# Kernel optimization log

Measured on AMD Instinct MI355X. Metric: run time of the kernel, lower is better.

Reference implementation:

```python
import jax, jax.numpy as jnp
import numpy as np

D, H, F, E, K = 1024, 16, 2048, 8, 2
EPS = 1e-5


def layernorm(x, g, b):
    m = jnp.mean(x, axis=-1, keepdims=True)
    v = jnp.mean((x - m) ** 2, axis=-1, keepdims=True)
    return (x - m) * jax.lax.rsqrt(v + EPS) * g + b


def mha(q_in, k_in, v_in, wq, wk, wv, bq, bk, bv, wo, bo):
    B, Tq, Dm = q_in.shape
    Tk = k_in.shape[1]
    dh = Dm // H
    q = (q_in @ wq + bq).reshape(B, Tq, H, dh)
    k = (k_in @ wk + bk).reshape(B, Tk, H, dh)
    v = (v_in @ wv + bv).reshape(B, Tk, H, dh)
    scores = jnp.einsum('bqhd,bkhd->bhqk', q, k) / jnp.sqrt(jnp.asarray(dh, q.dtype))
    attn = jax.nn.softmax(scores, axis=-1)
    out = jnp.einsum('bhqk,bkhd->bqhd', attn, v).reshape(B, Tq, Dm)
    return out @ wo + bo


def moe(x, rw, rb, w1, b1, w2, b2):
    B, T, Dm = x.shape
    xt = x.reshape(-1, Dm)                      # [N, D]
    N = xt.shape[0]
    logits = xt @ rw + rb                       # [N, E]
    probs = jax.nn.softmax(logits, axis=-1)
    topv, topi = jax.lax.top_k(probs, K)        # [N, K]
    gates = topv / jnp.sum(topv, axis=-1, keepdims=True)
    dense_gates = jnp.zeros((N, E), x.dtype).at[jnp.arange(N)[:, None], topi].set(gates)
    h = jax.nn.relu(jnp.einsum('td,edf->etf', xt, w1) + b1[:, None, :])  # [E, N, F]
    y = jnp.einsum('etf,efd->etd', h, w2) + b2[:, None, :]               # [E, N, D]
    out = jnp.einsum('te,etd->td', dense_gates, y).reshape(B, T, Dm)
    frac = jnp.mean(jnp.sum(jax.nn.one_hot(topi, E, dtype=x.dtype), axis=1) / K, axis=0)  # [E]
    importance = jnp.mean(probs, axis=0)        # [E]
    lb_loss = E * jnp.sum(frac * importance)
    return out, lb_loss


def forward(tgt, memory,
            sa_wq, sa_wk, sa_wv, sa_bq, sa_bk, sa_bv, sa_wo, sa_bo,
            ca_wq, ca_wk, ca_wv, ca_bq, ca_bk, ca_bv, ca_wo, ca_bo,
            ln1_g, ln1_b, ln2_g, ln2_b, ln3_g, ln3_b,
            rw, rb, w1, b1, w2, b2):
    t2 = mha(tgt, tgt, tgt, sa_wq, sa_wk, sa_wv, sa_bq, sa_bk, sa_bv, sa_wo, sa_bo)
    t = layernorm(tgt + t2, ln1_g, ln1_b)
    t2 = mha(t, memory, memory, ca_wq, ca_wk, ca_wv, ca_bq, ca_bk, ca_bv, ca_wo, ca_bo)
    t = layernorm(t + t2, ln2_g, ln2_b)
    t2, lb = moe(t, rw, rb, w1, b1, w2, b2)
    t = layernorm(t + t2, ln3_g, ln3_b)
    return t, lb


def setup_inputs() -> dict:
    key = jax.random.key(0)
    ks = jax.random.split(key, 24)
    s = 1.0 / np.sqrt(D)
    inp = {
        'tgt': jax.random.normal(ks[0], (4, 512, D), jnp.float32),
        'memory': jax.random.normal(ks[1], (4, 512, D), jnp.float32),
    }
    names = ['sa_wq', 'sa_wk', 'sa_wv', 'sa_wo', 'ca_wq', 'ca_wk', 'ca_wv', 'ca_wo']
    for i, n in enumerate(names):
        inp[n] = jax.random.normal(ks[2 + i], (D, D), jnp.float32) * s
    for n in ['sa_bq', 'sa_bk', 'sa_bv', 'sa_bo', 'ca_bq', 'ca_bk', 'ca_bv', 'ca_bo']:
        inp[n] = jnp.zeros((D,), jnp.float32)
    for n in ['ln1_g', 'ln2_g', 'ln3_g']:
        inp[n] = jnp.ones((D,), jnp.float32)
    for n in ['ln1_b', 'ln2_b', 'ln3_b']:
        inp[n] = jnp.zeros((D,), jnp.float32)
    inp['rw'] = jax.random.normal(ks[10], (D, E), jnp.float32) * s
    inp['rb'] = jnp.zeros((E,), jnp.float32)
    inp['w1'] = jax.random.normal(ks[11], (E, D, F), jnp.float32) * s
    inp['b1'] = jnp.zeros((E, F), jnp.float32)
    inp['w2'] = jax.random.normal(ks[12], (E, F, D), jnp.float32) * (1.0 / np.sqrt(F))
    inp['b2'] = jnp.zeros((E, D), jnp.float32)
    return inp


def reference(tgt, memory,
              sa_wq, sa_wk, sa_wv, sa_bq, sa_bk, sa_bv, sa_wo, sa_bo,
              ca_wq, ca_wk, ca_wv, ca_bq, ca_bk, ca_bv, ca_wo, ca_bo,
              ln1_g, ln1_b, ln2_g, ln2_b, ln3_g, ln3_b,
              rw, rb, w1, b1, w2, b2):
    return forward(tgt, memory,
                   sa_wq, sa_wk, sa_wv, sa_bq, sa_bk, sa_bv, sa_wo, sa_bo,
                   ca_wq, ca_wk, ca_wv, ca_bq, ca_bk, ca_bv, ca_wo, ca_bo,
                   ln1_g, ln1_b, ln2_g, ln2_b, ln3_g, ln3_b,
                   rw, rb, w1, b1, w2, b2)
```

## Files before the change

kernel.cpp:

```cpp
#include <hip/hip_runtime.h>

constexpr int Dm = 1024;
constexpr int NH = 16;
constexpr int Ff = 2048;
constexpr int NE = 8;
constexpr int Bn = 4;
constexpr int Tn = 512;
constexpr int Nt = 2048;

typedef float  f32x4  __attribute__((ext_vector_type(4)));
typedef __bf16 bf16x8 __attribute__((ext_vector_type(8)));
typedef unsigned short u16x8 __attribute__((ext_vector_type(8)));

__device__ inline unsigned short f2bf(float f) {
    unsigned u = __builtin_bit_cast(unsigned, f);
    u += 0x7FFFu + ((u >> 16) & 1u);
    return (unsigned short)(u >> 16);
}
__device__ inline float bf2f(unsigned short h) {
    unsigned u = (unsigned)h << 16;
    return __builtin_bit_cast(float, u);
}
__device__ inline void splitbf(float x, unsigned short& hi, unsigned short& lo) {
    hi = f2bf(x);
    lo = f2bf(x - bf2f(hi));
}
__device__ inline bf16x8 ld_frag(const unsigned short* p) {
    return __builtin_bit_cast(bf16x8, *(const u16x8*)p);
}

template <int SPLIT>
__global__ __launch_bounds__(256) void gemm_bf16_kernel(
    const float* __restrict__ A, int lda,
    const float* __restrict__ W0, const float* __restrict__ W1,
    const float* __restrict__ W2, int ldw, size_t weStride,
    const float* __restrict__ B0, const float* __restrict__ B1,
    const float* __restrict__ B2, size_t beStride,
    float* __restrict__ C, int ldc,
    int Mparam, int K,
    const int* __restrict__ lst, int lstStride, const int* __restrict__ cnt,
    int mode, int relu)
{
    __shared__ __align__(16) unsigned short AsH[128 * 40];
    __shared__ __align__(16) unsigned short WsH[128 * 40];
    __shared__ __align__(16) unsigned short AsL[SPLIT ? 128 * 40 : 1];
    __shared__ __align__(16) unsigned short WsL[SPLIT ? 128 * 40 : 1];
    __shared__ int inIdx[128];
    __shared__ int outIdx[128];

    const int e = blockIdx.z;
    const int M = (mode == 0) ? Mparam : cnt[e];
    const int m0 = blockIdx.y * 128;
    if (m0 >= M) return;
    const int n0 = blockIdx.x * 128;
    const int seg = n0 >> 10;
    const float* W = ((seg == 0) ? W0 : (seg == 1) ? W1 : W2) + (size_t)e * weStride;
    const float* bias = ((seg == 0) ? B0 : (seg == 1) ? B1 : B2) + (size_t)e * beStride;
    const int nseg = n0 & 1023;
    const int tid = threadIdx.x;

    if (tid < 128) {
        int g = m0 + tid;
        bool valid = g < M;
        int gi, go;
        if (mode == 0) { gi = valid ? g : (M - 1); go = valid ? g : -1; }
        else {
            int pid = lst[(size_t)e * lstStride + (valid ? g : 0)];
            gi = (mode == 1) ? (pid >> 1) : pid;
            go = valid ? pid : -1;
        }
        inIdx[tid] = gi;
        outIdx[tid] = go;
    }
    __syncthreads();

    const int ar = tid >> 1, ahalf = tid & 1;
    const int bn = (tid & 63) * 2, bko = ((tid >> 6) & 3) * 8;
    const float* aBase = A + (size_t)inIdx[ar] * lda + ahalf * 16;
    const float* wBase = W + (size_t)bko * ldw + nseg + bn;

    const int lane = tid & 63, wv = tid >> 6;
    const int wy = (wv >> 1) * 64, wx = (wv & 1) * 64;
    const int l15 = lane & 15, quad = lane >> 4;

    f32x4 acc[4][4];
    #pragma unroll
    for (int i = 0; i < 4; ++i)
        #pragma unroll
        for (int j = 0; j < 4; ++j) acc[i][j] = (f32x4)0.f;

    for (int k0 = 0; k0 < K; k0 += 32) {
        {
            const float* ap = aBase + k0;
            float v[16];
            *(float4*)&v[0]  = *(const float4*)(ap);
            *(float4*)&v[4]  = *(const float4*)(ap + 4);
            *(float4*)&v[8]  = *(const float4*)(ap + 8);
            *(float4*)&v[12] = *(const float4*)(ap + 12);
            u16x8 h0, h1, l0, l1;
            #pragma unroll
            for (int i = 0; i < 8; ++i) {
                unsigned short hh, ll;
                splitbf(v[i], hh, ll); h0[i] = hh; l0[i] = ll;
                splitbf(v[8 + i], hh, ll); h1[i] = hh; l1[i] = ll;
            }
            *(u16x8*)&AsH[ar * 40 + ahalf * 16]     = h0;
            *(u16x8*)&AsH[ar * 40 + ahalf * 16 + 8] = h1;
            if (SPLIT) {
                *(u16x8*)&AsL[ar * 40 + ahalf * 16]     = l0;
                *(u16x8*)&AsL[ar * 40 + ahalf * 16 + 8] = l1;
            }
        }
        {
            const float* wp = wBase + (size_t)k0 * ldw;
            float2 wr[8];
            #pragma unroll
            for (int j = 0; j < 8; ++j) wr[j] = *(const float2*)(wp + (size_t)j * ldw);
            u16x8 h0, h1, l0, l1;
            #pragma unroll
            for (int j = 0; j < 8; ++j) {
                unsigned short hh, ll;
                splitbf(wr[j].x, hh, ll); h0[j] = hh; l0[j] = ll;
                splitbf(wr[j].y, hh, ll); h1[j] = hh; l1[j] = ll;
            }
            *(u16x8*)&WsH[bn * 40 + bko]       = h0;
            *(u16x8*)&WsH[(bn + 1) * 40 + bko] = h1;
            if (SPLIT) {
                *(u16x8*)&WsL[bn * 40 + bko]       = l0;
                *(u16x8*)&WsL[(bn + 1) * 40 + bko] = l1;
            }
        }
        __syncthreads();
        bf16x8 ah[4], bh[4], al[4], bl[4];
        #pragma unroll
        for (int mi = 0; mi < 4; ++mi)
            ah[mi] = ld_frag(&AsH[(wy + mi * 16 + l15) * 40 + quad * 8]);
        #pragma unroll
        for (int ni = 0; ni < 4; ++ni)
            bh[ni] = ld_frag(&WsH[(wx + ni * 16 + l15) * 40 + quad * 8]);
        if (SPLIT) {
            #pragma unroll
            for (int mi = 0; mi < 4; ++mi)
                al[mi] = ld_frag(&AsL[(wy + mi * 16 + l15) * 40 + quad * 8]);
            #pragma unroll
            for (int ni = 0; ni < 4; ++ni)
                bl[ni] = ld_frag(&WsL[(wx + ni * 16 + l15) * 40 + quad * 8]);
        }
        #pragma unroll
        for (int mi = 0; mi < 4; ++mi)
            #pragma unroll
            for (int ni = 0; ni < 4; ++ni) {
                acc[mi][ni] = __builtin_amdgcn_mfma_f32_16x16x32_bf16(
                    ah[mi], bh[ni], acc[mi][ni], 0, 0, 0);
                if (SPLIT) {
                    acc[mi][ni] = __builtin_amdgcn_mfma_f32_16x16x32_bf16(
                        ah[mi], bl[ni], acc[mi][ni], 0, 0, 0);
                    acc[mi][ni] = __builtin_amdgcn_mfma_f32_16x16x32_bf16(
                        al[mi], bh[ni], acc[mi][ni], 0, 0, 0);
                }
            }
        __syncthreads();
    }

    #pragma unroll
    for (int mi = 0; mi < 4; ++mi) {
        #pragma unroll
        for (int r = 0; r < 4; ++r) {
            int rl = wy + mi * 16 + quad * 4 + r;
            int orow = outIdx[rl];
            if (orow < 0) continue;
            #pragma unroll
            for (int ni = 0; ni < 4; ++ni) {
                int col = n0 + wx + ni * 16 + l15;
                float val = acc[mi][ni][r] + bias[col & 1023];
                if (relu) val = fmaxf(val, 0.f);
                C[(size_t)orow * ldc + col] = val;
            }
        }
    }
}

__global__ __launch_bounds__(256) void attn_kernel(
    const float* __restrict__ Qp, int qld,
    const float* __restrict__ Kp, int kld, int kOff,
    const float* __restrict__ Vp, int vld, int vOff,
    float* __restrict__ O)
{
    __shared__ __align__(16) unsigned short KtH[64 * 72], KtL[64 * 72];
    __shared__ __align__(16) unsigned short VtH[64 * 72], VtL[64 * 72];
    __shared__ __align__(16) unsigned short PtH[4][16 * 72], PtL[4][16 * 72];

    const int tid = threadIdx.x, lane = tid & 63, wv = tid >> 6;
    const int quad = lane >> 4, l15 = lane & 15;
    const int b = blockIdx.z, h = blockIdx.y, q0 = blockIdx.x * 64;
    const int bT = b * Tn;

    bf16x8 aqh[2], aql[2];
    {
        const float* qp = Qp + (size_t)(bT + q0 + wv * 16 + l15) * qld + h * 64;
        #pragma unroll
        for (int s = 0; s < 2; ++s) {
            float v[8];
            *(float4*)&v[0] = *(const float4*)(qp + s * 32 + quad * 8);
            *(float4*)&v[4] = *(const float4*)(qp + s * 32 + quad * 8 + 4);
            u16x8 th, tl;
            #pragma unroll
            for (int i = 0; i < 8; ++i) {
                unsigned short hh, ll;
                splitbf(v[i], hh, ll); th[i] = hh; tl[i] = ll;
            }
            aqh[s] = __builtin_bit_cast(bf16x8, th);
            aql[s] = __builtin_bit_cast(bf16x8, tl);
        }
    }

    f32x4 oacc[4];
    #pragma unroll
    for (int i = 0; i < 4; ++i) oacc[i] = (f32x4)0.f;
    float mrow[4] = {-1e30f, -1e30f, -1e30f, -1e30f};
    float lrow[4] = {0.f, 0.f, 0.f, 0.f};

    const int rr = tid >> 2, cc = tid & 3;

    for (int kt0 = 0; kt0 < Tn; kt0 += 64) {
        {
            const float* kr = Kp + (size_t)(bT + kt0 + rr) * kld + kOff + h * 64 + cc * 16;
            float v[16];
            *(float4*)&v[0]  = *(const float4*)(kr);
            *(float4*)&v[4]  = *(const float4*)(kr + 4);
            *(float4*)&v[8]  = *(const float4*)(kr + 8);
            *(float4*)&v[12] = *(const float4*)(kr + 12);
            u16x8 h0, h1, l0, l1;
            #pragma unroll
            for (int i = 0; i < 8; ++i) {
                unsigned short hh, ll;
                splitbf(v[i], hh, ll); h0[i] = hh; l0[i] = ll;
                splitbf(v[8 + i], hh, ll); h1[i] = hh; l1[i] = ll;
            }
            *(u16x8*)&KtH[rr * 72 + cc * 16]     = h0;
            *(u16x8*)&KtH[rr * 72 + cc * 16 + 8] = h1;
            *(u16x8*)&KtL[rr * 72 + cc * 16]     = l0;
            *(u16x8*)&KtL[rr * 72 + cc * 16 + 8] = l1;

            const float* vr = Vp + (size_t)(bT + kt0 + rr) * vld + vOff + h * 64 + cc * 16;
            float fv[16];
            *(float4*)&fv[0]  = *(const float4*)(vr);
            *(float4*)&fv[4]  = *(const float4*)(vr + 4);
            *(float4*)&fv[8]  = *(const float4*)(vr + 8);
            *(float4*)&fv[12] = *(const float4*)(vr + 12);
            #pragma unroll
            for (int i = 0; i < 16; ++i) {
                unsigned short hh, ll;
                splitbf(fv[i], hh, ll);
                VtH[(cc * 16 + i) * 72 + rr] = hh;
                VtL[(cc * 16 + i) * 72 + rr] = ll;
            }
        }
        __syncthreads();

        f32x4 sacc[4];
        #pragma unroll
        for (int nt = 0; nt < 4; ++nt) {
            sacc[nt] = (f32x4)0.f;
            #pragma unroll
            for (int s = 0; s < 2; ++s) {
                bf16x8 bkh = ld_frag(&KtH[(nt * 16 + l15) * 72 + s * 32 + quad * 8]);
                bf16x8 bkl = ld_frag(&KtL[(nt * 16 + l15) * 72 + s * 32 + quad * 8]);
                sacc[nt] = __builtin_amdgcn_mfma_f32_16x16x32_bf16(aqh[s], bkh, sacc[nt], 0, 0, 0);
                sacc[nt] = __builtin_amdgcn_mfma_f32_16x16x32_bf16(aqh[s], bkl, sacc[nt], 0, 0, 0);
                sacc[nt] = __builtin_amdgcn_mfma_f32_16x16x32_bf16(aql[s], bkh, sacc[nt], 0, 0, 0);
            }
        }
        #pragma unroll
        for (int nt = 0; nt < 4; ++nt)
            #pragma unroll
            for (int r = 0; r < 4; ++r) sacc[nt][r] *= 0.125f;

        float alpha[4], mnew[4];
        #pragma unroll
        for (int r = 0; r < 4; ++r) {
            float mx = fmaxf(fmaxf(sacc[0][r], sacc[1][r]), fmaxf(sacc[2][r], sacc[3][r]));
            #pragma unroll
            for (int msk = 1; msk < 16; msk <<= 1) mx = fmaxf(mx, __shfl_xor(mx, msk));
            mnew[r] = fmaxf(mrow[r], mx);
            alpha[r] = __expf(mrow[r] - mnew[r]);
            mrow[r] = mnew[r];
        }
        float rs[4] = {0.f, 0.f, 0.f, 0.f};
        #pragma unroll
        for (int nt = 0; nt < 4; ++nt)
            #pragma unroll
            for (int r = 0; r < 4; ++r) {
                float p = __expf(sacc[nt][r] - mnew[r]);
                sacc[nt][r] = p;
                rs[r] += p;
            }
        #pragma unroll
        for (int r = 0; r < 4; ++r) {
            #pragma unroll
            for (int msk = 1; msk < 16; msk <<= 1) rs[r] += __shfl_xor(rs[r], msk);
            lrow[r] = lrow[r] * alpha[r] + rs[r];
        }
        #pragma unroll
        for (int ni = 0; ni < 4; ++ni)
            #pragma unroll
            for (int r = 0; r < 4; ++r) oacc[ni][r] *= alpha[r];

        #pragma unroll
        for (int nt = 0; nt < 4; ++nt)
            #pragma unroll
            for (int r = 0; r < 4; ++r) {
                unsigned short hh, ll;
                splitbf(sacc[nt][r], hh, ll);
                PtH[wv][(quad * 4 + r) * 72 + nt * 16 + l15] = hh;
                PtL[wv][(quad * 4 + r) * 72 + nt * 16 + l15] = ll;
            }
        asm volatile("s_waitcnt lgkmcnt(0)" ::: "memory");

        #pragma unroll
        for (int s = 0; s < 2; ++s) {
            bf16x8 aph = ld_frag(&PtH[wv][l15 * 72 + s * 32 + quad * 8]);
            bf16x8 apl = ld_frag(&PtL[wv][l15 * 72 + s * 32 + quad * 8]);
            #pragma unroll
            for (int ni = 0; ni < 4; ++ni) {
                bf16x8 bvh = ld_frag(&VtH[(ni * 16 + l15) * 72 + s * 32 + quad * 8]);
                bf16x8 bvl = ld_frag(&VtL[(ni * 16 + l15) * 72 + s * 32 + quad * 8]);
                oacc[ni] = __builtin_amdgcn_mfma_f32_16x16x32_bf16(aph, bvh, oacc[ni], 0, 0, 0);
                oacc[ni] = __builtin_amdgcn_mfma_f32_16x16x32_bf16(aph, bvl, oacc[ni], 0, 0, 0);
                oacc[ni] = __builtin_amdgcn_mfma_f32_16x16x32_bf16(apl, bvh, oacc[ni], 0, 0, 0);
            }
        }
        __syncthreads();
    }

    #pragma unroll
    for (int r = 0; r < 4; ++r) {
        float inv = 1.f / lrow[r];
        int orow = bT + q0 + wv * 16 + quad * 4 + r;
        #pragma unroll
        for (int ni = 0; ni < 4; ++ni) {
            int col = h * 64 + ni * 16 + l15;
            O[(size_t)orow * Dm + col] = oacc[ni][r] * inv;
        }
    }
}

__global__ __launch_bounds__(256) void ln_residual_kernel(
    const float* __restrict__ X, const float* __restrict__ R,
    const float* __restrict__ g, const float* __restrict__ bta,
    float* __restrict__ Out)
{
    __shared__ float red[8];
    const int t = blockIdx.x, tid = threadIdx.x;
    float v[4];
    float s = 0.f;
    #pragma unroll
    for (int i = 0; i < 4; ++i) {
        int c = tid + i * 256;
        v[i] = X[(size_t)t * Dm + c] + R[(size_t)t * Dm + c];
        s += v[i];
    }
    #pragma unroll
    for (int off = 32; off; off >>= 1) s += __shfl_down(s, off);
    const int wid = tid >> 6;
    if ((tid & 63) == 0) red[wid] = s;
    __syncthreads();
    const float mean = (red[0] + red[1] + red[2] + red[3]) * (1.f / 1024.f);
    float s2 = 0.f;
    #pragma unroll
    for (int i = 0; i < 4; ++i) { float d = v[i] - mean; s2 += d * d; }
    #pragma unroll
    for (int off = 32; off; off >>= 1) s2 += __shfl_down(s2, off);
    if ((tid & 63) == 0) red[4 + wid] = s2;
    __syncthreads();
    const float var  = (red[4] + red[5] + red[6] + red[7]) * (1.f / 1024.f);
    const float rstd = rsqrtf(var + 1e-5f);
    #pragma unroll
    for (int i = 0; i < 4; ++i) {
        int c = tid + i * 256;
        Out[(size_t)t * Dm + c] = (v[i] - mean) * rstd * g[c] + bta[c];
    }
}

constexpr int RT_TPB = 32;
__global__ __launch_bounds__(256) void router_kernel(
    const float* __restrict__ X, const float* __restrict__ rw,
    const float* __restrict__ rb, float* __restrict__ gatep,
    int* __restrict__ elist, int* __restrict__ ecnt,
    float* __restrict__ impf, float* __restrict__ cntf)
{
    __shared__ float simp[NE];
    __shared__ int   scnt[NE];
    __shared__ int   sbase[NE];
    __shared__ int   sexp[RT_TPB][2];
    __shared__ int   spos[RT_TPB][2];

    const int tid = threadIdx.x, lane = tid & 63, wv = tid >> 6;
    if (tid < NE) { simp[tid] = 0.f; scnt[tid] = 0; }
    __syncthreads();

    const int t0 = blockIdx.x * RT_TPB;

    for (int i = 0; i < 8; ++i) {
        const int slot = wv * 8 + i;
        const int t = t0 + slot;
        float l[NE];
        #pragma unroll
        for (int e = 0; e < NE; ++e) l[e] = 0.f;
        #pragma unroll
        for (int j = 0; j < Dm / 64; ++j) {
            int d = lane + j * 64;
            float x = X[(size_t)t * Dm + d];
            #pragma unroll
            for (int e = 0; e < NE; ++e) l[e] += x * rw[d * NE + e];
        }
        #pragma unroll
        for (int e = 0; e < NE; ++e) {
            float vv = l[e];
            #pragma unroll
            for (int off = 32; off; off >>= 1) vv += __shfl_down(vv, off);
            l[e] = vv;
        }
        if (lane == 0) {
            float mx = -1e30f;
            #pragma unroll
            for (int e = 0; e < NE; ++e) { l[e] += rb[e]; mx = fmaxf(mx, l[e]); }
            float p[NE];
            float sum = 0.f;
            #pragma unroll
            for (int e = 0; e < NE; ++e) { p[e] = __expf(l[e] - mx); sum += p[e]; }
            const float inv = 1.f / sum;
            int e0 = 0, e1 = 0;
            float v0 = -1.f, v1 = -1.f;
            #pragma unroll
            for (int e = 0; e < NE; ++e) {
                float pe = p[e] * inv;
                atomicAdd(&simp[e], pe);
                if (pe > v0)      { v1 = v0; e1 = e0; v0 = pe; e0 = e; }
                else if (pe > v1) { v1 = pe; e1 = e; }
            }
            const float gs = 1.f / (v0 + v1);
            sexp[slot][0] = e0;
            sexp[slot][1] = e1;
            spos[slot][0] = atomicAdd(&scnt[e0], 1);
            spos[slot][1] = atomicAdd(&scnt[e1], 1);
            gatep[2 * t]     = v0 * gs;
            gatep[2 * t + 1] = v1 * gs;
        }
    }
    __syncthreads();

    if (tid < NE) {
        sbase[tid] = atomicAdd(&ecnt[tid], scnt[tid]);
        atomicAdd(&impf[tid], simp[tid]);
        atomicAdd(&cntf[tid], (float)scnt[tid]);
    }
    __syncthreads();

    if (tid < RT_TPB * 2) {
        const int slot = tid >> 1, k = tid & 1;
        const int e = sexp[slot][k];
        elist[e * Nt + sbase[e] + spos[slot][k]] = 2 * (t0 + slot) + k;
    }
}

__global__ void init_kernel(int* ecnt, float* impf, float* cntf)
{
    int i = threadIdx.x;
    if (i < NE) { ecnt[i] = 0; impf[i] = 0.f; cntf[i] = 0.f; }
}

__global__ void lb_kernel(const float* __restrict__ impf,
                          const float* __restrict__ cntf,
                          float* __restrict__ out)
{
    if (threadIdx.x == 0) {
        float s = 0.f;
        for (int e = 0; e < NE; ++e) s += cntf[e] * impf[e];
        out[0] = (float)NE * s / ((float)Nt * 2.f * (float)Nt);
    }
}

__global__ __launch_bounds__(256) void moe_combine(
    const float* __restrict__ Y, const float* __restrict__ gatep,
    float* __restrict__ Out)
{
    int i = blockIdx.x * 256 + threadIdx.x;
    int t = i >> 10, c = i & 1023;
    Out[i] = gatep[2 * t] * Y[(size_t)(2 * t) * Dm + c]
           + gatep[2 * t + 1] * Y[(size_t)(2 * t + 1) * Dm + c];
}

extern "C" void kernel_launch(void* const* d_in, const int* in_sizes, int n_in,
                              void* d_out, int out_size, void* d_ws, size_t ws_size,
                              hipStream_t stream)
{
    const float* tgt   = (const float*)d_in[0];
    const float* memry = (const float*)d_in[1];
    const float* sa_wq = (const float*)d_in[2];
    const float* sa_wk = (const float*)d_in[3];
    const float* sa_wv = (const float*)d_in[4];
    const float* sa_wo = (const float*)d_in[5];
    const float* ca_wq = (const float*)d_in[6];
    const float* ca_wk = (const float*)d_in[7];
    const float* ca_wv = (const float*)d_in[8];
    const float* ca_wo = (const float*)d_in[9];
    const float* sa_bq = (const float*)d_in[10];
    const float* sa_bk = (const float*)d_in[11];
    const float* sa_bv = (const float*)d_in[12];
    const float* sa_bo = (const float*)d_in[13];
    const float* ca_bq = (const float*)d_in[14];
    const float* ca_bk = (const float*)d_in[15];
    const float* ca_bv = (const float*)d_in[16];
    const float* ca_bo = (const float*)d_in[17];
    const float* ln1_g = (const float*)d_in[18];
    const float* ln2_g = (const float*)d_in[19];
    const float* ln3_g = (const float*)d_in[20];
    const float* ln1_b = (const float*)d_in[21];
    const float* ln2_b = (const float*)d_in[22];
    const float* ln3_b = (const float*)d_in[23];
    const float* rw    = (const float*)d_in[24];
    const float* rb    = (const float*)d_in[25];
    const float* w1    = (const float*)d_in[26];
    const float* b1    = (const float*)d_in[27];
    const float* w2    = (const float*)d_in[28];
    const float* b2    = (const float*)d_in[29];

    float* ws = (float*)d_ws;
    const size_t ND = (size_t)Nt * Dm;
    float* qkv  = ws;
    float* qc   = ws;
    float* kvc  = ws + ND;
    float* attnO = ws + 3 * ND;
    float* hbuf = ws;
    float* t2   = ws + 4 * ND;
    float* tb   = ws + 5 * ND;
    float* ybuf = ws + 6 * ND;
    float* gatep = ws + 8 * ND;
    int*   elist = (int*)(gatep + 2 * Nt);
    int*   ecnt  = elist + NE * Nt;
    float* impf  = (float*)(ecnt + NE);
    float* cntf  = impf + NE;
    float* outp  = (float*)d_out;

    dim3 blk(256);
    dim3 attnGrid(Tn / 64, NH, Bn);

    gemm_bf16_kernel<1><<<dim3(24, 16, 1), blk, 0, stream>>>(
        tgt, Dm, sa_wq, sa_wk, sa_wv, Dm, 0, sa_bq, sa_bk, sa_bv, 0,
        qkv, 3 * Dm, Nt, Dm, nullptr, 0, nullptr, 0, 0);
    attn_kernel<<<attnGrid, blk, 0, stream>>>(
        qkv, 3 * Dm, qkv, 3 * Dm, 1024, qkv, 3 * Dm, 2048, attnO);
    gemm_bf16_kernel<1><<<dim3(8, 16, 1), blk, 0, stream>>>(
        attnO, Dm, sa_wo, sa_wo, sa_wo, Dm, 0, sa_bo, sa_bo, sa_bo, 0,
        t2, Dm, Nt, Dm, nullptr, 0, nullptr, 0, 0);
    ln_residual_kernel<<<Nt, blk, 0, stream>>>(tgt, t2, ln1_g, ln1_b, tb);

    gemm_bf16_kernel<1><<<dim3(8, 16, 1), blk, 0, stream>>>(
        tb, Dm, ca_wq, ca_wq, ca_wq, Dm, 0, ca_bq, ca_bq, ca_bq, 0,
        qc, Dm, Nt, Dm, nullptr, 0, nullptr, 0, 0);
    gemm_bf16_kernel<1><<<dim3(16, 16, 1), blk, 0, stream>>>(
        memry, Dm, ca_wk, ca_wv, ca_wv, Dm, 0, ca_bk, ca_bv, ca_bv, 0,
        kvc, 2 * Dm, Nt, Dm, nullptr, 0, nullptr, 0, 0);
    attn_kernel<<<attnGrid, blk, 0, stream>>>(
        qc, Dm, kvc, 2 * Dm, 0, kvc, 2 * Dm, 1024, attnO);
    gemm_bf16_kernel<1><<<dim3(8, 16, 1), blk, 0, stream>>>(
        attnO, Dm, ca_wo, ca_wo, ca_wo, Dm, 0, ca_bo, ca_bo, ca_bo, 0,
        t2, Dm, Nt, Dm, nullptr, 0, nullptr, 0, 0);
    ln_residual_kernel<<<Nt, blk, 0, stream>>>(tb, t2, ln2_g, ln2_b, tb);

    init_kernel<<<1, 64, 0, stream>>>(ecnt, impf, cntf);
    router_kernel<<<Nt / RT_TPB, blk, 0, stream>>>(tb, rw, rb, gatep, elist, ecnt, impf, cntf);
    gemm_bf16_kernel<1><<<dim3(16, 16, 8), blk, 0, stream>>>(
        tb, Dm, w1, w1 + 1024, w1 + 1024, Ff, (size_t)Dm * Ff, b1, b1 + 1024, b1 + 1024, Ff,
        hbuf, Ff, 0, Dm, elist, Nt, ecnt, 1, 1);
    gemm_bf16_kernel<1><<<dim3(8, 16, 8), blk, 0, stream>>>(
        hbuf, Ff, w2, w2, w2, Dm, (size_t)Ff * Dm, b2, b2, b2, Dm,
        ybuf, Dm, 0, Ff, elist, Nt, ecnt, 2, 0);
    moe_combine<<<(Nt * Dm) / 256, blk, 0, stream>>>(ybuf, gatep, t2);
    ln_residual_kernel<<<Nt, blk, 0, stream>>>(tb, t2, ln3_g, ln3_b, outp);
    lb_kernel<<<1, 64, 0, stream>>>(impf, cntf, outp + ND);
}
```

Measured before the change: 896.0 us.

## Pre-split operands to bf16 hi/lo, use direct LDS loads, fuse MoE combine

```diff
diff --git a/kernel.cpp b/kernel.cpp
--- a/kernel.cpp
+++ b/kernel.cpp
@@ -10,41 +10,52 @@
 
 typedef float  f32x4  __attribute__((ext_vector_type(4)));
 typedef __bf16 bf16x8 __attribute__((ext_vector_type(8)));
-typedef unsigned short u16x8 __attribute__((ext_vector_type(8)));
-
-__device__ inline unsigned short f2bf(float f) {
+typedef unsigned short u16;
+typedef u16 u16x8v __attribute__((ext_vector_type(8)));
+typedef u16 u16x4v __attribute__((ext_vector_type(4)));
+
+__device__ inline u16 f2bf(float f) {
     unsigned u = __builtin_bit_cast(unsigned, f);
     u += 0x7FFFu + ((u >> 16) & 1u);
-    return (unsigned short)(u >> 16);
-}
-__device__ inline float bf2f(unsigned short h) {
+    return (u16)(u >> 16);
+}
+__device__ inline float bf2f(u16 h) {
     unsigned u = (unsigned)h << 16;
     return __builtin_bit_cast(float, u);
 }
-__device__ inline void splitbf(float x, unsigned short& hi, unsigned short& lo) {
+__device__ inline void splitbf(float x, u16& hi, u16& lo) {
     hi = f2bf(x);
     lo = f2bf(x - bf2f(hi));
 }
-__device__ inline bf16x8 ld_frag(const unsigned short* p) {
-    return __builtin_bit_cast(bf16x8, *(const u16x8*)p);
-}
-
-template <int SPLIT>
-__global__ __launch_bounds__(256) void gemm_bf16_kernel(
-    const float* __restrict__ A, int lda,
-    const float* __restrict__ W0, const float* __restrict__ W1,
-    const float* __restrict__ W2, int ldw, size_t weStride,
+__device__ inline bf16x8 ld_frag(const u16* p) {
+    return __builtin_bit_cast(bf16x8, *(const u16x8v*)p);
+}
+__device__ inline void cp16(const u16* g, u16* l) {
+    __builtin_amdgcn_global_load_lds(
+        (const __attribute__((address_space(1))) unsigned int*)g,
+        (__attribute__((address_space(3))) unsigned int*)l, 16, 0, 0);
+}
+
+template <int SPLIT, int CMODE>
+__global__ __launch_bounds__(256) void gemm_kernel(
+    const u16* __restrict__ Ahi, const u16* __restrict__ Alo, int lda,
+    const u16* __restrict__ Whi, const u16* __restrict__ Wlo, size_t weStride,
     const float* __restrict__ B0, const float* __restrict__ B1,
     const float* __restrict__ B2, size_t beStride,
-    float* __restrict__ C, int ldc,
+    void* __restrict__ C0, void* __restrict__ C1, int ldc,
     int Mparam, int K,
     const int* __restrict__ lst, int lstStride, const int* __restrict__ cnt,
-    int mode, int relu)
-{
-    __shared__ __align__(16) unsigned short AsH[128 * 40];
-    __shared__ __align__(16) unsigned short WsH[128 * 40];
-    __shared__ __align__(16) unsigned short AsL[SPLIT ? 128 * 40 : 1];
-    __shared__ __align__(16) unsigned short WsL[SPLIT ? 128 * 40 : 1];
+    int mode, int relu,
+    const u16* __restrict__ A2hi, const u16* __restrict__ A2lo, int lda2,
+    const u16* __restrict__ W2hi, const u16* __restrict__ W2lo,
+    const float* __restrict__ B20, const float* __restrict__ B21,
+    void* __restrict__ C20, void* __restrict__ C21, int ldc2, int xSplit,
+    const float* __restrict__ gatep, float* __restrict__ accOut)
+{
+    __shared__ __align__(16) u16 AsH[128 * 32];
+    __shared__ __align__(16) u16 WsH[128 * 32];
+    __shared__ __align__(16) u16 AsL[SPLIT ? 128 * 32 : 8];
+    __shared__ __align__(16) u16 WsL[SPLIT ? 128 * 32 : 8];
     __shared__ int inIdx[128];
     __shared__ int outIdx[128];
 
@@ -52,11 +63,21 @@
     const int M = (mode == 0) ? Mparam : cnt[e];
     const int m0 = blockIdx.y * 128;
     if (m0 >= M) return;
-    const int n0 = blockIdx.x * 128;
-    const int seg = n0 >> 10;
-    const float* W = ((seg == 0) ? W0 : (seg == 1) ? W1 : W2) + (size_t)e * weStride;
-    const float* bias = ((seg == 0) ? B0 : (seg == 1) ? B1 : B2) + (size_t)e * beStride;
-    const int nseg = n0 & 1023;
+
+    int bx = blockIdx.x;
+    const u16 *aH = Ahi, *aL = Alo, *wH = Whi, *wL = Wlo;
+    const float *b0 = B0, *b1 = B1, *b2 = B2;
+    void *c0 = C0, *c1 = C1;
+    int myLda = lda, myLdc = ldc;
+    if (xSplit && bx >= xSplit) {
+        bx -= xSplit;
+        aH = A2hi; aL = A2lo; wH = W2hi; wL = W2lo;
+        b0 = B20; b1 = B21; b2 = B21;
+        c0 = C20; c1 = C21; myLda = lda2; myLdc = ldc2;
+    }
+    const int n0 = bx * 128;
+    const int seg = n0 >> 10, nseg = n0 & 1023;
+    const float* bias = ((seg == 0) ? b0 : (seg == 1) ? b1 : b2) + (size_t)e * beStride;
     const int tid = threadIdx.x;
 
     if (tid < 128) {
@@ -74,12 +95,32 @@
     }
     __syncthreads();
 
-    const int ar = tid >> 1, ahalf = tid & 1;
-    const int bn = (tid & 63) * 2, bko = ((tid >> 6) & 3) * 8;
-    const float* aBase = A + (size_t)inIdx[ar] * lda + ahalf * 16;
-    const float* wBase = W + (size_t)bko * ldw + nseg + bn;
-
     const int lane = tid & 63, wv = tid >> 6;
+    const int c0i = wv * 2, c1i = wv * 2 + 1;
+    const int r0 = c0i * 16 + (lane >> 2), r1 = c1i * 16 + (lane >> 2);
+    const int kc0 = (lane & 3) ^ ((r0 >> 1) & 3);
+    const int kc1 = (lane & 3) ^ ((r1 >> 1) & 3);
+    const size_t wOff = (size_t)e * weStride;
+    const u16* aH0 = aH + (size_t)inIdx[r0] * myLda + kc0 * 8;
+    const u16* aH1 = aH + (size_t)inIdx[r1] * myLda + kc1 * 8;
+    const u16* wH0 = wH + wOff + (size_t)(n0 + r0) * K + kc0 * 8;
+    const u16* wH1 = wH + wOff + (size_t)(n0 + r1) * K + kc1 * 8;
+    const u16 *aL0 = nullptr, *aL1 = nullptr, *wL0 = nullptr, *wL1 = nullptr;
+    if (SPLIT) {
+        aL0 = aL + (size_t)inIdx[r0] * myLda + kc0 * 8;
+        aL1 = aL + (size_t)inIdx[r1] * myLda + kc1 * 8;
+        wL0 = wL + wOff + (size_t)(n0 + r0) * K + kc0 * 8;
+        wL1 = wL + wOff + (size_t)(n0 + r1) * K + kc1 * 8;
+    }
+    u16* ldsA0 = &AsH[c0i * 512];
+    u16* ldsA1 = &AsH[c1i * 512];
+    u16* ldsW0 = &WsH[c0i * 512];
+    u16* ldsW1 = &WsH[c1i * 512];
+    u16* ldsAL0 = SPLIT ? &AsL[c0i * 512] : nullptr;
+    u16* ldsAL1 = SPLIT ? &AsL[c1i * 512] : nullptr;
+    u16* ldsWL0 = SPLIT ? &WsL[c0i * 512] : nullptr;
+    u16* ldsWL1 = SPLIT ? &WsL[c1i * 512] : nullptr;
+
     const int wy = (wv >> 1) * 64, wx = (wv & 1) * 64;
     const int l15 = lane & 15, quad = lane >> 4;
 
@@ -90,61 +131,32 @@
         for (int j = 0; j < 4; ++j) acc[i][j] = (f32x4)0.f;
 
     for (int k0 = 0; k0 < K; k0 += 32) {
-        {
-            const float* ap = aBase + k0;
-            float v[16];
-            *(float4*)&v[0]  = *(const float4*)(ap);
-            *(float4*)&v[4]  = *(const float4*)(ap + 4);
-            *(float4*)&v[8]  = *(const float4*)(ap + 8);
-            *(float4*)&v[12] = *(const float4*)(ap + 12);
-            u16x8 h0, h1, l0, l1;
-            #pragma unroll
-            for (int i = 0; i < 8; ++i) {
-                unsigned short hh, ll;
-                splitbf(v[i], hh, ll); h0[i] = hh; l0[i] = ll;
-                splitbf(v[8 + i], hh, ll); h1[i] = hh; l1[i] = ll;
-            }
-            *(u16x8*)&AsH[ar * 40 + ahalf * 16]     = h0;
-            *(u16x8*)&AsH[ar * 40 + ahalf * 16 + 8] = h1;
-            if (SPLIT) {
-                *(u16x8*)&AsL[ar * 40 + ahalf * 16]     = l0;
-                *(u16x8*)&AsL[ar * 40 + ahalf * 16 + 8] = l1;
-            }
-        }
-        {
-            const float* wp = wBase + (size_t)k0 * ldw;
-            float2 wr[8];
-            #pragma unroll
-            for (int j = 0; j < 8; ++j) wr[j] = *(const float2*)(wp + (size_t)j * ldw);
-            u16x8 h0, h1, l0, l1;
-            #pragma unroll
-            for (int j = 0; j < 8; ++j) {
-                unsigned short hh, ll;
-                splitbf(wr[j].x, hh, ll); h0[j] = hh; l0[j] = ll;
-                splitbf(wr[j].y, hh, ll); h1[j] = hh; l1[j] = ll;
-            }
-            *(u16x8*)&WsH[bn * 40 + bko]       = h0;
-            *(u16x8*)&WsH[(bn + 1) * 40 + bko] = h1;
-            if (SPLIT) {
-                *(u16x8*)&WsL[bn * 40 + bko]       = l0;
-                *(u16x8*)&WsL[(bn + 1) * 40 + bko] = l1;
-            }
+        cp16(aH0 + k0, ldsA0);
+        cp16(aH1 + k0, ldsA1);
+        cp16(wH0 + k0, ldsW0);
+        cp16(wH1 + k0, ldsW1);
+        if (SPLIT) {
+            cp16(aL0 + k0, ldsAL0);
+            cp16(aL1 + k0, ldsAL1);
+            cp16(wL0 + k0, ldsWL0);
+            cp16(wL1 + k0, ldsWL1);
         }
         __syncthreads();
+
         bf16x8 ah[4], bh[4], al[4], bl[4];
         #pragma unroll
-        for (int mi = 0; mi < 4; ++mi)
-            ah[mi] = ld_frag(&AsH[(wy + mi * 16 + l15) * 40 + quad * 8]);
-        #pragma unroll
-        for (int ni = 0; ni < 4; ++ni)
-            bh[ni] = ld_frag(&WsH[(wx + ni * 16 + l15) * 40 + quad * 8]);
-        if (SPLIT) {
-            #pragma unroll
-            for (int mi = 0; mi < 4; ++mi)
-                al[mi] = ld_frag(&AsL[(wy + mi * 16 + l15) * 40 + quad * 8]);
-            #pragma unroll
-            for (int ni = 0; ni < 4; ++ni)
-                bl[ni] = ld_frag(&WsL[(wx + ni * 16 + l15) * 40 + quad * 8]);
+        for (int mi = 0; mi < 4; ++mi) {
+            int r = wy + mi * 16 + l15;
+            int sl = quad ^ ((r >> 1) & 3);
+            ah[mi] = ld_frag(&AsH[r * 32 + sl * 8]);
+            if (SPLIT) al[mi] = ld_frag(&AsL[r * 32 + sl * 8]);
+        }
+        #pragma unroll
+        for (int ni = 0; ni < 4; ++ni) {
+            int r = wx + ni * 16 + l15;
+            int sl = quad ^ ((r >> 1) & 3);
+            bh[ni] = ld_frag(&WsH[r * 32 + sl * 8]);
+            if (SPLIT) bl[ni] = ld_frag(&WsL[r * 32 + sl * 8]);
         }
         #pragma unroll
         for (int mi = 0; mi < 4; ++mi)
@@ -171,24 +183,37 @@
             if (orow < 0) continue;
             #pragma unroll
             for (int ni = 0; ni < 4; ++ni) {
-                int col = n0 + wx + ni * 16 + l15;
-                float val = acc[mi][ni][r] + bias[col & 1023];
+                int col = nseg + wx + ni * 16 + l15;
+                float val = acc[mi][ni][r] + bias[col];
                 if (relu) val = fmaxf(val, 0.f);
-                C[(size_t)orow * ldc + col] = val;
+                int gcol = n0 + wx + ni * 16 + l15;
+                if (CMODE == 3) {
+                    atomicAdd(&accOut[(size_t)(orow >> 1) * Dm + gcol],
+                              gatep[orow] * val);
+                } else if (CMODE == 2) {
+                    u16 hh, ll;
+                    splitbf(val, hh, ll);
+                    ((u16*)c0)[(size_t)orow * myLdc + gcol] = hh;
+                    ((u16*)c1)[(size_t)orow * myLdc + gcol] = ll;
+                } else if (CMODE == 1) {
+                    ((u16*)c0)[(size_t)orow * myLdc + gcol] = f2bf(val);
+                } else {
+                    ((float*)c0)[(size_t)orow * myLdc + gcol] = val;
+                }
             }
         }
     }
 }
 
 __global__ __launch_bounds__(256) void attn_kernel(
-    const float* __restrict__ Qp, int qld,
-    const float* __restrict__ Kp, int kld, int kOff,
-    const float* __restrict__ Vp, int vld, int vOff,
-    float* __restrict__ O)
-{
-    __shared__ __align__(16) unsigned short KtH[64 * 72], KtL[64 * 72];
-    __shared__ __align__(16) unsigned short VtH[64 * 72], VtL[64 * 72];
-    __shared__ __align__(16) unsigned short PtH[4][16 * 72], PtL[4][16 * 72];
+    const u16* __restrict__ QH, const u16* __restrict__ QL, int qld, int qOff,
+    const u16* __restrict__ KH, const u16* __restrict__ KL, int kld, int kOff,
+    const u16* __restrict__ VH, const u16* __restrict__ VL, int vld, int vOff,
+    u16* __restrict__ OH, u16* __restrict__ OL)
+{
+    __shared__ __align__(16) u16 KtH[64 * 72], KtL[64 * 72];
+    __shared__ __align__(16) u16 VtH[64 * 72], VtL[64 * 72];
+    __shared__ __align__(16) u16 PtH[4][16 * 72], PtL[4][16 * 72];
 
     const int tid = threadIdx.x, lane = tid & 63, wv = tid >> 6;
     const int quad = lane >> 4, l15 = lane & 15;
@@ -197,20 +222,11 @@
 
     bf16x8 aqh[2], aql[2];
     {
-        const float* qp = Qp + (size_t)(bT + q0 + wv * 16 + l15) * qld + h * 64;
+        size_t qbase = (size_t)(bT + q0 + wv * 16 + l15) * qld + qOff + h * 64;
         #pragma unroll
         for (int s = 0; s < 2; ++s) {
-            float v[8];
-            *(float4*)&v[0] = *(const float4*)(qp + s * 32 + quad * 8);
-            *(float4*)&v[4] = *(const float4*)(qp + s * 32 + quad * 8 + 4);
-            u16x8 th, tl;
-            #pragma unroll
-            for (int i = 0; i < 8; ++i) {
-                unsigned short hh, ll;
-                splitbf(v[i], hh, ll); th[i] = hh; tl[i] = ll;
-            }
-            aqh[s] = __builtin_bit_cast(bf16x8, th);
-            aql[s] = __builtin_bit_cast(bf16x8, tl);
+            aqh[s] = ld_frag(QH + qbase + s * 32 + quad * 8);
+            aql[s] = ld_frag(QL + qbase + s * 32 + quad * 8);
         }
     }
 
@@ -224,36 +240,23 @@
 
     for (int kt0 = 0; kt0 < Tn; kt0 += 64) {
         {
-            const float* kr = Kp + (size_t)(bT + kt0 + rr) * kld + kOff + h * 64 + cc * 16;
-            float v[16];
-            *(float4*)&v[0]  = *(const float4*)(kr);
-            *(float4*)&v[4]  = *(const float4*)(kr + 4);
-            *(float4*)&v[8]  = *(const float4*)(kr + 8);
-            *(float4*)&v[12] = *(const float4*)(kr + 12);
-            u16x8 h0, h1, l0, l1;
+            size_t kb = (size_t)(bT + kt0 + rr) * kld + kOff + h * 64 + cc * 16;
+            *(u16x8v*)&KtH[rr * 72 + cc * 16]     = *(const u16x8v*)(KH + kb);
+            *(u16x8v*)&KtH[rr * 72 + cc * 16 + 8] = *(const u16x8v*)(KH + kb + 8);
+            *(u16x8v*)&KtL[rr * 72 + cc * 16]     = *(const u16x8v*)(KL + kb);
+            *(u16x8v*)&KtL[rr * 72 + cc * 16 + 8] = *(const u16x8v*)(KL + kb + 8);
+
+            size_t vb = (size_t)(bT + kt0 + rr) * vld + vOff + h * 64 + cc * 16;
+            u16x8v va = *(const u16x8v*)(VH + vb);
+            u16x8v vbv = *(const u16x8v*)(VH + vb + 8);
+            u16x8v la = *(const u16x8v*)(VL + vb);
+            u16x8v lb = *(const u16x8v*)(VL + vb + 8);
             #pragma unroll
             for (int i = 0; i < 8; ++i) {
-                unsigned short hh, ll;
-                splitbf(v[i], hh, ll); h0[i] = hh; l0[i] = ll;
-                splitbf(v[8 + i], hh, ll); h1[i] = hh; l1[i] = ll;
-            }
-            *(u16x8*)&KtH[rr * 72 + cc * 16]     = h0;
-            *(u16x8*)&KtH[rr * 72 + cc * 16 + 8] = h1;
-            *(u16x8*)&KtL[rr * 72 + cc * 16]     = l0;
-            *(u16x8*)&KtL[rr * 72 + cc * 16 + 8] = l1;
-
-            const float* vr = Vp + (size_t)(bT + kt0 + rr) * vld + vOff + h * 64 + cc * 16;
-            float fv[16];
-            *(float4*)&fv[0]  = *(const float4*)(vr);
-            *(float4*)&fv[4]  = *(const float4*)(vr + 4);
-            *(float4*)&fv[8]  = *(const float4*)(vr + 8);
-            *(float4*)&fv[12] = *(const float4*)(vr + 12);
-            #pragma unroll
-            for (int i = 0; i < 16; ++i) {
-                unsigned short hh, ll;
-                splitbf(fv[i], hh, ll);
-                VtH[(cc * 16 + i) * 72 + rr] = hh;
-                VtL[(cc * 16 + i) * 72 + rr] = ll;
+                VtH[(cc * 16 + i) * 72 + rr]     = va[i];
+                VtH[(cc * 16 + 8 + i) * 72 + rr] = vbv[i];
+                VtL[(cc * 16 + i) * 72 + rr]     = la[i];
+                VtL[(cc * 16 + 8 + i) * 72 + rr] = lb[i];
             }
         }
         __syncthreads();
@@ -310,7 +313,7 @@
         for (int nt = 0; nt < 4; ++nt)
             #pragma unroll
             for (int r = 0; r < 4; ++r) {
-                unsigned short hh, ll;
+                u16 hh, ll;
                 splitbf(sacc[nt][r], hh, ll);
                 PtH[wv][(quad * 4 + r) * 72 + nt * 16 + l15] = hh;
                 PtL[wv][(quad * 4 + r) * 72 + nt * 16 + l15] = ll;
@@ -340,7 +343,10 @@
         #pragma unroll
         for (int ni = 0; ni < 4; ++ni) {
             int col = h * 64 + ni * 16 + l15;
-            O[(size_t)orow * Dm + col] = oacc[ni][r] * inv;
+            u16 hh, ll;
+            splitbf(oacc[ni][r] * inv, hh, ll);
+            OH[(size_t)orow * Dm + col] = hh;
+            OL[(size_t)orow * Dm + col] = ll;
         }
     }
 }
@@ -348,7 +354,7 @@
 __global__ __launch_bounds__(256) void ln_residual_kernel(
     const float* __restrict__ X, const float* __restrict__ R,
     const float* __restrict__ g, const float* __restrict__ bta,
-    float* __restrict__ Out)
+    float* __restrict__ Out, u16* __restrict__ outH, u16* __restrict__ outL)
 {
     __shared__ float red[8];
     const int t = blockIdx.x, tid = threadIdx.x;
@@ -378,7 +384,54 @@
     #pragma unroll
     for (int i = 0; i < 4; ++i) {
         int c = tid + i * 256;
-        Out[(size_t)t * Dm + c] = (v[i] - mean) * rstd * g[c] + bta[c];
+        float o = (v[i] - mean) * rstd * g[c] + bta[c];
+        Out[(size_t)t * Dm + c] = o;
+        if (outH) {
+            u16 hh, ll;
+            splitbf(o, hh, ll);
+            outH[(size_t)t * Dm + c] = hh;
+            outL[(size_t)t * Dm + c] = ll;
+        }
+    }
+}
+
+__global__ __launch_bounds__(256) void split_kernel(
+    const float* __restrict__ src, u16* __restrict__ hi, u16* __restrict__ lo)
+{
+    int i = (blockIdx.x * 256 + threadIdx.x) * 4;
+    float4 v = *(const float4*)(src + i);
+    u16x4v h, l;
+    u16 hh, ll;
+    splitbf(v.x, hh, ll); h[0] = hh; l[0] = ll;
+    splitbf(v.y, hh, ll); h[1] = hh; l[1] = ll;
+    splitbf(v.z, hh, ll); h[2] = hh; l[2] = ll;
+    splitbf(v.w, hh, ll); h[3] = hh; l[3] = ll;
+    *(u16x4v*)(hi + i) = h;
+    *(u16x4v*)(lo + i) = l;
+}
+
+__global__ __launch_bounds__(256) void wT_kernel(
+    const float* __restrict__ src, size_t srcEStride, int Ksrc, int Nsrc,
+    u16* __restrict__ dhi, u16* __restrict__ dlo, size_t dstEStride)
+{
+    __shared__ float tile[64][65];
+    const int e = blockIdx.z;
+    src += (size_t)e * srcEStride;
+    dhi += (size_t)e * dstEStride;
+    if (dlo) dlo += (size_t)e * dstEStride;
+    const int n0 = blockIdx.x * 64, k0 = blockIdx.y * 64;
+    for (int i = threadIdx.x; i < 4096; i += 256) {
+        int r = i >> 6, c = i & 63;
+        tile[r][c] = src[(size_t)(k0 + r) * Nsrc + n0 + c];
+    }
+    __syncthreads();
+    for (int i = threadIdx.x; i < 4096; i += 256) {
+        int r = i >> 6, c = i & 63;
+        float v = tile[c][r];
+        u16 hh, ll;
+        splitbf(v, hh, ll);
+        dhi[(size_t)(n0 + r) * Ksrc + k0 + c] = hh;
+        if (dlo) dlo[(size_t)(n0 + r) * Ksrc + k0 + c] = ll;
     }
 }
 
@@ -464,10 +517,17 @@
     }
 }
 
-__global__ void init_kernel(int* ecnt, float* impf, float* cntf)
-{
-    int i = threadIdx.x;
-    if (i < NE) { ecnt[i] = 0; impf[i] = 0.f; cntf[i] = 0.f; }
+__global__ __launch_bounds__(256) void zero_kernel(
+    float* __restrict__ t2, int* __restrict__ ecnt,
+    float* __restrict__ impf, float* __restrict__ cntf)
+{
+    int i = blockIdx.x * 256 + threadIdx.x;
+    *(float4*)&t2[(size_t)i * 4] = make_float4(0.f, 0.f, 0.f, 0.f);
+    if (blockIdx.x == 0 && threadIdx.x < NE) {
+        ecnt[threadIdx.x] = 0;
+        impf[threadIdx.x] = 0.f;
+        cntf[threadIdx.x] = 0.f;
+    }
 }
 
 __global__ void lb_kernel(const float* __restrict__ impf,
@@ -479,16 +539,6 @@
         for (int e = 0; e < NE; ++e) s += cntf[e] * impf[e];
         out[0] = (float)NE * s / ((float)Nt * 2.f * (float)Nt);
     }
-}
-
-__global__ __launch_bounds__(256) void moe_combine(
-    const float* __restrict__ Y, const float* __restrict__ gatep,
-    float* __restrict__ Out)
-{
-    int i = blockIdx.x * 256 + threadIdx.x;
-    int t = i >> 10, c = i & 1023;
-    Out[i] = gatep[2 * t] * Y[(size_t)(2 * t) * Dm + c]
-           + gatep[2 * t + 1] * Y[(size_t)(2 * t + 1) * Dm + c];
 }
 
 extern "C" void kernel_launch(void* const* d_in, const int* in_sizes, int n_in,
@@ -526,17 +576,30 @@
     const float* w2    = (const float*)d_in[28];
     const float* b2    = (const float*)d_in[29];
 
-    float* ws = (float*)d_ws;
     const size_t ND = (size_t)Nt * Dm;
-    float* qkv  = ws;
-    float* qc   = ws;
-    float* kvc  = ws + ND;
-    float* attnO = ws + 3 * ND;
-    float* hbuf = ws;
-    float* t2   = ws + 4 * ND;
-    float* tb   = ws + 5 * ND;
-    float* ybuf = ws + 6 * ND;
-    float* gatep = ws + 8 * ND;
+    const size_t MM = (size_t)1024 * 1024;
+    u16* U = (u16*)d_ws;
+    size_t off = 0;
+    auto A = [&](size_t n) { u16* p = U + off; off += n; return p; };
+    u16* qkvT_h  = A(3 * MM);  u16* qkvT_l  = A(3 * MM);
+    u16* cakvT_h = A(2 * MM);  u16* cakvT_l = A(2 * MM);
+    u16* caqT_h  = A(MM);      u16* caqT_l  = A(MM);
+    u16* saoT_h  = A(MM);      u16* saoT_l  = A(MM);
+    u16* caoT_h  = A(MM);      u16* caoT_l  = A(MM);
+    u16* w1t     = A(16 * MM);
+    u16* w2t     = A(16 * MM);
+    u16* tgtH = A(ND);  u16* tgtL = A(ND);
+    u16* memH = A(ND);  u16* memL = A(ND);
+    u16* qkvH = A(3 * ND);  u16* qkvL = A(3 * ND);
+    u16* kvcH = A(2 * ND);  u16* kvcL = A(2 * ND);
+    u16* tbH  = A(ND);  u16* tbL = A(ND);
+    u16* qcH = tgtH, *qcL = tgtL;
+    u16* aoH = memH, *aoL = memL;
+    u16* hbuf = qkvH;
+    float* Fp = (float*)(U + off);
+    float* t2 = Fp;
+    float* tb = Fp + ND;
+    float* gatep = tb + ND;
     int*   elist = (int*)(gatep + 2 * Nt);
     int*   ecnt  = elist + NE * Nt;
     float* impf  = (float*)(ecnt + NE);
@@ -545,39 +608,63 @@
 
     dim3 blk(256);
     dim3 attnGrid(Tn / 64, NH, Bn);
-
-    gemm_bf16_kernel<1><<<dim3(24, 16, 1), blk, 0, stream>>>(
-        tgt, Dm, sa_wq, sa_wk, sa_wv, Dm, 0, sa_bq, sa_bk, sa_bv, 0,
-        qkv, 3 * Dm, Nt, Dm, nullptr, 0, nullptr, 0, 0);
+    dim3 wtG(16, 16, 1);
+
+    split_kernel<<<ND / 1024, blk, 0, stream>>>(tgt, tgtH, tgtL);
+    split_kernel<<<ND / 1024, blk, 0, stream>>>(memry, memH, memL);
+    wT_kernel<<<wtG, blk, 0, stream>>>(sa_wq, 0, 1024, 1024, qkvT_h,          qkvT_l,          0);
+    wT_kernel<<<wtG, blk, 0, stream>>>(sa_wk, 0, 1024, 1024, qkvT_h + MM,     qkvT_l + MM,     0);
+    wT_kernel<<<wtG, blk, 0, stream>>>(sa_wv, 0, 1024, 1024, qkvT_h + 2 * MM, qkvT_l + 2 * MM, 0);
+    wT_kernel<<<wtG, blk, 0, stream>>>(ca_wk, 0, 1024, 1024, cakvT_h,         cakvT_l,         0);
+    wT_kernel<<<wtG, blk, 0, stream>>>(ca_wv, 0, 1024, 1024, cakvT_h + MM,    cakvT_l + MM,    0);
+    wT_kernel<<<wtG, blk, 0, stream>>>(ca_wq, 0, 1024, 1024, caqT_h, caqT_l, 0);
+    wT_kernel<<<wtG, blk, 0, stream>>>(sa_wo, 0, 1024, 1024, saoT_h, saoT_l, 0);
+    wT_kernel<<<wtG, blk, 0, stream>>>(ca_wo, 0, 1024, 1024, caoT_h, caoT_l, 0);
+    wT_kernel<<<dim3(32, 16, 8), blk, 0, stream>>>(w1, 2 * MM, 1024, 2048, w1t, nullptr, 2 * MM);
+    wT_kernel<<<dim3(16, 32, 8), blk, 0, stream>>>(w2, 2 * MM, 2048, 1024, w2t, nullptr, 2 * MM);
+
+    gemm_kernel<1, 2><<<dim3(40, 16, 1), blk, 0, stream>>>(
+        tgtH, tgtL, 1024, qkvT_h, qkvT_l, 0, sa_bq, sa_bk, sa_bv, 0,
+        qkvH, qkvL, 3072, Nt, 1024, nullptr, 0, nullptr, 0, 0,
+        memH, memL, 1024, cakvT_h, cakvT_l, ca_bk, ca_bv,
+        kvcH, kvcL, 2048, 24, nullptr, nullptr);
     attn_kernel<<<attnGrid, blk, 0, stream>>>(
-        qkv, 3 * Dm, qkv, 3 * Dm, 1024, qkv, 3 * Dm, 2048, attnO);
-    gemm_bf16_kernel<1><<<dim3(8, 16, 1), blk, 0, stream>>>(
-        attnO, Dm, sa_wo, sa_wo, sa_wo, Dm, 0, sa_bo, sa_bo, sa_bo, 0,
-        t2, Dm, Nt, Dm, nullptr, 0, nullptr, 0, 0);
-    ln_residual_kernel<<<Nt, blk, 0, stream>>>(tgt, t2, ln1_g, ln1_b, tb);
-
-    gemm_bf16_kernel<1><<<dim3(8, 16, 1), blk, 0, stream>>>(
-        tb, Dm, ca_wq, ca_wq, ca_wq, Dm, 0, ca_bq, ca_bq, ca_bq, 0,
-        qc, Dm, Nt, Dm, nullptr, 0, nullptr, 0, 0);
-    gemm_bf16_kernel<1><<<dim3(16, 16, 1), blk, 0, stream>>>(
-        memry, Dm, ca_wk, ca_wv, ca_wv, Dm, 0, ca_bk, ca_bv, ca_bv, 0,
-        kvc, 2 * Dm, Nt, Dm, nullptr, 0, nullptr, 0, 0);
+        qkvH, qkvL, 3072, 0, qkvH, qkvL, 3072, 1024, qkvH, qkvL, 3072, 2048,
+        aoH, aoL);
+    gemm_kernel<1, 0><<<dim3(8, 16, 1), blk, 0, stream>>>(
+        aoH, aoL, 1024, saoT_h, saoT_l, 0, sa_bo, sa_bo, sa_bo, 0,
+        t2, nullptr, 1024, Nt, 1024, nullptr, 0, nullptr, 0, 0,
+        nullptr, nullptr, 0, nullptr, nullptr, nullptr, nullptr,
+        nullptr, nullptr, 0, 0, nullptr, nullptr);
+    ln_residual_kernel<<<Nt, blk, 0, stream>>>(tgt, t2, ln1_g, ln1_b, tb, tbH, tbL);
+
+    gemm_kernel<1, 2><<<dim3(8, 16, 1), blk, 0, stream>>>(
+        tbH, tbL, 1024, caqT_h, caqT_l, 0, ca_bq, ca_bq, ca_bq, 0,
+        qcH, qcL, 1024, Nt, 1024, nullptr, 0, nullptr, 0, 0,
+        nullptr, nullptr, 0, nullptr, nullptr, nullptr, nullptr,
+        nullptr, nullptr, 0, 0, nullptr, nullptr);
     attn_kernel<<<attnGrid, blk, 0, stream>>>(
-        qc, Dm, kvc, 2 * Dm, 0, kvc, 2 * Dm, 1024, attnO);
-    gemm_bf16_kernel<1><<<dim3(8, 16, 1), blk, 0, stream>>>(
-        attnO, Dm, ca_wo, ca_wo, ca_wo, Dm, 0, ca_bo, ca_bo, ca_bo, 0,
-        t2, Dm, Nt, Dm, nullptr, 0, nullptr, 0, 0);
-    ln_residual_kernel<<<Nt, blk, 0, stream>>>(tb, t2, ln2_g, ln2_b, tb);
-
-    init_kernel<<<1, 64, 0, stream>>>(ecnt, impf, cntf);
+        qcH, qcL, 1024, 0, kvcH, kvcL, 2048, 0, kvcH, kvcL, 2048, 1024,
+        aoH, aoL);
+    gemm_kernel<1, 0><<<dim3(8, 16, 1), blk, 0, stream>>>(
+        aoH, aoL, 1024, caoT_h, caoT_l, 0, ca_bo, ca_bo, ca_bo, 0,
+        t2, nullptr, 1024, Nt, 1024, nullptr, 0, nullptr, 0, 0,
+        nullptr, nullptr, 0, nullptr, nullptr, nullptr, nullptr,
+        nullptr, nullptr, 0, 0, nullptr, nullptr);
+    ln_residual_kernel<<<Nt, blk, 0, stream>>>(tb, t2, ln2_g, ln2_b, tb, tbH, tbL);
+
+    zero_kernel<<<(Nt * Dm) / 1024, blk, 0, stream>>>(t2, ecnt, impf, cntf);
     router_kernel<<<Nt / RT_TPB, blk, 0, stream>>>(tb, rw, rb, gatep, elist, ecnt, impf, cntf);
-    gemm_bf16_kernel<1><<<dim3(16, 16, 8), blk, 0, stream>>>(
-        tb, Dm, w1, w1 + 1024, w1 + 1024, Ff, (size_t)Dm * Ff, b1, b1 + 1024, b1 + 1024, Ff,
-        hbuf, Ff, 0, Dm, elist, Nt, ecnt, 1, 1);
-    gemm_bf16_kernel<1><<<dim3(8, 16, 8), blk, 0, stream>>>(
-        hbuf, Ff, w2, w2, w2, Dm, (size_t)Ff * Dm, b2, b2, b2, Dm,
-        ybuf, Dm, 0, Ff, elist, Nt, ecnt, 2, 0);
-    moe_combine<<<(Nt * Dm) / 256, blk, 0, stream>>>(ybuf, gatep, t2);
-    ln_residual_kernel<<<Nt, blk, 0, stream>>>(tb, t2, ln3_g, ln3_b, outp);
+    gemm_kernel<0, 1><<<dim3(16, 16, 8), blk, 0, stream>>>(
+        tbH, nullptr, 1024, w1t, nullptr, 2 * MM, b1, b1 + 1024, b1 + 1024, Ff,
+        hbuf, nullptr, 2048, 0, 1024, elist, Nt, ecnt, 1, 1,
+        nullptr, nullptr, 0, nullptr, nullptr, nullptr, nullptr,
+        nullptr, nullptr, 0, 0, nullptr, nullptr);
+    gemm_kernel<0, 3><<<dim3(8, 16, 8), blk, 0, stream>>>(
+        hbuf, nullptr, 2048, w2t, nullptr, 2 * MM, b2, b2, b2, Dm,
+        nullptr, nullptr, 1024, 0, 2048, elist, Nt, ecnt, 2, 0,
+        nullptr, nullptr, 0, nullptr, nullptr, nullptr, nullptr,
+        nullptr, nullptr, 0, 0, gatep, t2);
+    ln_residual_kernel<<<Nt, blk, 0, stream>>>(tb, t2, ln3_g, ln3_b, outp, nullptr, nullptr);
     lb_kernel<<<1, 64, 0, stream>>>(impf, cntf, outp + ND);
 }
```

New measurement: 790.3 us. 1.13x faster.
